# Kernel tuning notes

Hardware: AMD Instinct MI355X
Metric: run time of the kernel (lower is better)

## Reference

```python
import jax, jax.numpy as jnp
import numpy as np

D_MODEL = 1024
EXPAND = 2
D_INNER = D_MODEL * EXPAND  # 2048
C = 8
B, T = 4, 2048


def setup_inputs() -> dict:
    key = jax.random.key(0)
    ks = jax.random.split(key, 8)
    x = jax.random.normal(ks[0], (B, T, D_MODEL), jnp.float32)
    # omega init: uniform in [a, b] per the torch code
    a = np.log(1.0 / np.exp(np.log(0.999) / C) - 1.0)
    b = np.log(1.0 / np.exp(np.log(0.9) / C) - 1.0)
    omega = (a + (b - a) * jax.random.uniform(ks[1], (1, 1, D_INNER))).astype(jnp.float32)
    s = 0.02
    Win = (jax.random.normal(ks[2], (2 * D_INNER, D_MODEL)) * s).astype(jnp.float32)   # in_proj, no bias
    Wl = (jax.random.normal(ks[3], (D_INNER, D_INNER)) * s).astype(jnp.float32)        # lambda_proj weight
    bl = jnp.zeros((D_INNER,), jnp.float32)                                            # lambda_proj bias
    Wv = (jax.random.normal(ks[4], (D_INNER, D_INNER)) * s).astype(jnp.float32)        # mixer householder-vector proj
    bv = jnp.zeros((D_INNER,), jnp.float32)
    Wout = (jax.random.normal(ks[5], (D_MODEL, D_INNER)) * s).astype(jnp.float32)      # out_proj, no bias
    return dict(x=x, omega=omega, Win=Win, Wl=Wl, bl=bl, Wv=Wv, bv=bv, Wout=Wout)


def reference(x, omega, Win, Wl, bl, Wv, bv, Wout):
    # in_proj then split into (x, z)
    xz = jnp.einsum('btd,ed->bte', x, Win)              # [B,T,2*D_INNER]
    xi, z = jnp.split(xz, 2, axis=-1)                   # each [B,T,D_INNER]
    # lambda gate (computed for all timesteps at once)
    log_lam = -C * jax.nn.softplus(omega) * jax.nn.sigmoid(jnp.einsum('bti,ji->btj', xi, Wl) + bl)
    lam = jnp.exp(log_lam)                              # [B,T,D_INNER]
    # Householder (rank-1, identity activation) mixer vectors, hoisted out of the scan
    v = jnp.einsum('bti,ji->btj', xi, Wv) + bv          # [B,T,D_INNER]

    h0 = xi[:, 0]                                       # [B,D_INNER]

    def step(h_prev, inp):
        x_t, v_t, lam_t = inp
        vh = jnp.sum(v_t * h_prev, axis=-1, keepdims=True)
        vv = jnp.sum(v_t * v_t, axis=-1, keepdims=True)
        Qh = h_prev - 2.0 * v_t * (vh / vv)             # Householder reflection of h
        h = lam_t * Qh + (1.0 - lam_t) * x_t
        return h, h

    xs = (jnp.swapaxes(xi[:, 1:], 0, 1),                # [T-1,B,D_INNER]
          jnp.swapaxes(v[:, 1:], 0, 1),
          jnp.swapaxes(lam[:, 1:], 0, 1))
    _, hs = jax.lax.scan(step, h0, xs)                  # [T-1,B,D_INNER]
    h = jnp.concatenate([h0[:, None], jnp.swapaxes(hs, 0, 1)], axis=1)  # [B,T,D_INNER]

    return jnp.einsum('bti,di->btd', jax.nn.silu(z) * h, Wout)
```

## Files before the change

### kernel.cpp

```cpp
#include <hip/hip_runtime.h>
#include <cstdint>
#include <cstddef>

typedef unsigned short u16;
typedef __attribute__((ext_vector_type(8))) short s8v;
typedef __attribute__((ext_vector_type(4))) float f4v;
typedef __attribute__((ext_vector_type(2))) float f32x2;

#define D_MODEL 1024
#define D_INNER 2048
#define BT      8192
#define TLEN    2048
#define NBATCH  4

struct alignas(8) U16x4 { u16 x, y, z, w; };

__device__ __forceinline__ u16 f2bf(float f) {
  union { float f; unsigned u; } c; c.f = f;
  unsigned r = c.u + 0x7FFFu + ((c.u >> 16) & 1u);
  return (u16)(r >> 16);
}
__device__ __forceinline__ float blo(unsigned u) {
  union { unsigned u; float f; } c; c.u = u << 16; return c.f;
}
__device__ __forceinline__ float bhi(unsigned u) {
  union { unsigned u; float f; } c; c.u = u & 0xffff0000u; return c.f;
}
__device__ __forceinline__ unsigned pkbf(float lo, float hi) {
  union { float f; unsigned u; } a, b; a.f = lo; b.f = hi;
#if __has_builtin(__builtin_amdgcn_perm)
  return __builtin_amdgcn_perm(b.u + 0x8000u, a.u + 0x8000u, 0x07060302u);
#else
  return ((b.u + 0x8000u) & 0xffff0000u) | ((a.u + 0x8000u) >> 16);
#endif
}

#define DPPADD(x, ctrl) \
  ((x) + __builtin_bit_cast(float, __builtin_amdgcn_update_dpp( \
       0, __builtin_bit_cast(int, (x)), (ctrl), 0xF, 0xF, true)))
__device__ __forceinline__ float wave_sum_dpp(float x) {
  x = DPPADD(x, 0x111);
  x = DPPADD(x, 0x112);
  x = DPPADD(x, 0x114);
  x = DPPADD(x, 0x118);
  x = DPPADD(x, 0x142);
  x = DPPADD(x, 0x143);
  return x;
}

__device__ __forceinline__ void glds16(const u16* g, const u16* lds) {
  __builtin_amdgcn_global_load_lds(
      (const __attribute__((address_space(1))) unsigned int*)(uintptr_t)g,
      (__attribute__((address_space(3))) unsigned int*)(unsigned int)(uintptr_t)lds,
      16, 0, 0);
}

template<int EPI>
__global__ __launch_bounds__(256, 2)
void gemm_nt(const u16* __restrict__ A, const u16* __restrict__ B,
             int M, int N, int K,
             float* __restrict__ Cf, u16* __restrict__ Cb, u16* __restrict__ Cb2,
             const float* __restrict__ bias, const float* __restrict__ sfac,
             const float* __restrict__ bias2)
{
  __shared__ u16 lA[128 * 32];
  __shared__ u16 lB[128 * 32];
  const int tid  = threadIdx.x;
  const int wave = tid >> 6, lane = tid & 63;
  const int wm = wave >> 1, wn = wave & 1;

  const int nwg = (int)(gridDim.x * gridDim.y);
  int wg = (int)(blockIdx.y * gridDim.x + blockIdx.x);
  wg = (wg & 7) * (nwg >> 3) + (wg >> 3);
  const int bm0 = (wg / (int)gridDim.x) * 128;
  const int bn0 = (wg % (int)gridDim.x) * 128;

  const int srow = lane >> 2;
  const int scol = (lane & 3) * 8;
  const u16* pa0 = A + (size_t)(bm0 + wave * 32 + srow) * K + scol;
  const u16* pa1 = pa0 + (size_t)16 * K;
  const u16* pb0 = B + (size_t)(bn0 + wave * 32 + srow) * K + scol;
  const u16* pb1 = pb0 + (size_t)16 * K;
  u16* la0 = lA + (wave * 32) * 32;
  u16* la1 = la0 + 16 * 32;
  u16* lb0 = lB + (wave * 32) * 32;
  u16* lb1 = lb0 + 16 * 32;

  const int fr = lane & 15, kq = lane >> 4;
  const u16* fA = lA + (wm * 64 + fr) * 32 + kq * 8;
  const u16* fB = lB + (wn * 64 + fr) * 32 + kq * 8;

  f4v acc[4][4];
  const f4v zf = {0.f, 0.f, 0.f, 0.f};
  for (int i = 0; i < 4; ++i)
    for (int j = 0; j < 4; ++j)
      acc[i][j] = zf;

  for (int k0 = 0; k0 < K; k0 += 32) {
    glds16(pa0 + k0, la0);
    glds16(pa1 + k0, la1);
    glds16(pb0 + k0, lb0);
    glds16(pb1 + k0, lb1);
    __syncthreads();
    s8v af[4], bfv[4];
#pragma unroll
    for (int i = 0; i < 4; ++i) af[i] = *(const s8v*)(fA + i * 16 * 32);
#pragma unroll
    for (int j = 0; j < 4; ++j) bfv[j] = *(const s8v*)(fB + j * 16 * 32);
#pragma unroll
    for (int i = 0; i < 4; ++i)
#pragma unroll
      for (int j = 0; j < 4; ++j)
        acc[i][j] = __builtin_amdgcn_mfma_f32_16x16x32_bf16(af[i], bfv[j], acc[i][j], 0, 0, 0);
    __syncthreads();
  }

#pragma unroll
  for (int i = 0; i < 4; ++i) {
#pragma unroll
    for (int j = 0; j < 4; ++j) {
#pragma unroll
      for (int r = 0; r < 4; ++r) {
        const int gm = bm0 + wm * 64 + i * 16 + kq * 4 + r;
        const int gn = bn0 + wn * 64 + j * 16 + fr;
        const float val = acc[i][j][r];
        if (EPI == 0) {
          if (gn < D_INNER) {
            Cb[(size_t)gm * D_INNER + gn] = f2bf(val);
          } else {
            const float s = val / (1.f + __expf(-val));
            Cb2[(size_t)gm * D_INNER + (gn - D_INNER)] = f2bf(s);
          }
        } else if (EPI == 4) {
          if (gn < D_INNER) {
            const float pre = val + bias[gn];
            const float sig = 1.f / (1.f + __expf(-pre));
            const float m = -expm1f(sfac[gn] * sig);
            Cb2[(size_t)gm * D_INNER + gn] = f2bf(m);
          } else {
            Cb[(size_t)gm * D_INNER + (gn - D_INNER)] = f2bf(val + bias2[gn - D_INNER]);
          }
        } else {
          Cf[(size_t)gm * N + gn] = val;
        }
      }
    }
  }
}

#define CV_R0 2097152
#define CV_R1 3145728
#define CV_R2 4194304
#define CV_R3 5242880
#define CV_R4 5767168

__global__ __launch_bounds__(256)
void convall_kernel(const float* __restrict__ x, const float* __restrict__ Win,
                    const float* __restrict__ Wl, const float* __restrict__ Wv,
                    const float* __restrict__ Wout, u16* __restrict__ outb)
{
  const int g = blockIdx.x * 256 + threadIdx.x;
  const float* in; int lo;
  if (g < CV_R0)      { in = x;    lo = g; }
  else if (g < CV_R1) { in = Win;  lo = g - CV_R0; }
  else if (g < CV_R2) { in = Wl;   lo = g - CV_R1; }
  else if (g < CV_R3) { in = Wv;   lo = g - CV_R2; }
  else                { in = Wout; lo = g - CV_R3; }
  const float4 v = ((const float4*)in)[lo];
  U16x4 o; o.x = f2bf(v.x); o.y = f2bf(v.y); o.z = f2bf(v.z); o.w = f2bf(v.w);
  ((U16x4*)outb)[g] = o;
}

__global__ void sfac_kernel(const float* __restrict__ omega, float* __restrict__ sfac)
{
  const int i = blockIdx.x * blockDim.x + threadIdx.x;
  if (i < D_INNER) sfac[i] = -8.f * log1pf(expf(omega[i]));
}

__global__ __launch_bounds__(256)
void vscale_kernel(u16* __restrict__ v)
{
  const int row  = blockIdx.x * 4 + (threadIdx.x >> 6);
  const int lane = threadIdx.x & 63;
  uint4* p = (uint4*)(v + (size_t)row * D_INNER + lane * 32);
  uint4 a[4];
#pragma unroll
  for (int i = 0; i < 4; ++i) a[i] = p[i];
  float s = 0.f;
#pragma unroll
  for (int i = 0; i < 4; ++i) {
    const unsigned w[4] = {a[i].x, a[i].y, a[i].z, a[i].w};
#pragma unroll
    for (int j = 0; j < 4; ++j) {
      const float f0 = blo(w[j]), f1 = bhi(w[j]);
      s += f0 * f0 + f1 * f1;
    }
  }
  s += __shfl_down(s, 32); s += __shfl_down(s, 16); s += __shfl_down(s, 8);
  s += __shfl_down(s, 4);  s += __shfl_down(s, 2);  s += __shfl_down(s, 1);
  const float sc = sqrtf(2.f / __shfl(s, 0));
#pragma unroll
  for (int i = 0; i < 4; ++i) {
    const unsigned w[4] = {a[i].x, a[i].y, a[i].z, a[i].w};
    unsigned o[4];
#pragma unroll
    for (int j = 0; j < 4; ++j) o[j] = pkbf(blo(w[j]) * sc, bhi(w[j]) * sc);
    uint4 ov; ov.x = o[0]; ov.y = o[1]; ov.z = o[2]; ov.w = o[3];
    p[i] = ov;
  }
}

__global__ __launch_bounds__(256)
void pairprep_kernel(const u16* __restrict__ vs, const u16* __restrict__ mb,
                     const u16* __restrict__ xi, f32x2* __restrict__ C12)
{
  const int r = blockIdx.x * 4 + (threadIdx.x >> 6);
  const int lane = threadIdx.x & 63;
  const int b = r >> 10;
  const int t = (r & 1023) * 2;
  const size_t o0 = ((size_t)b * TLEN + t) * D_INNER + (size_t)lane * 32;
  const size_t o1 = o0 + D_INNER;
  const uint4* pv0 = (const uint4*)(vs + o0);
  const uint4* pv1 = (const uint4*)(vs + o1);
  const uint4* px0 = (const uint4*)(xi + o0);
  const uint4* pm0 = (const uint4*)(mb + o0);
  float c1 = 0.f, c2 = 0.f;
#pragma unroll
  for (int i = 0; i < 4; ++i) {
    const uint4 v0 = pv0[i], v1 = pv1[i], x0 = px0[i], m0 = pm0[i];
    const unsigned v0w[4] = {v0.x, v0.y, v0.z, v0.w};
    const unsigned v1w[4] = {v1.x, v1.y, v1.z, v1.w};
    const unsigned x0w[4] = {x0.x, x0.y, x0.z, x0.w};
    const unsigned m0w[4] = {m0.x, m0.y, m0.z, m0.w};
#pragma unroll
    for (int q = 0; q < 4; ++q) {
      const float va = blo(v0w[q]), vb = bhi(v0w[q]);
      const float ua = blo(v1w[q]), ub = bhi(v1w[q]);
      const float xa = blo(x0w[q]), xb = bhi(x0w[q]);
      const float ma = blo(m0w[q]), mbv = bhi(m0w[q]);
      const float wa = __builtin_fmaf(-ua, ma, ua);
      const float wb = __builtin_fmaf(-ub, mbv, ub);
      c1 += wa * va + wb * vb;
      c2 += ua * (ma * xa) + ub * (mbv * xb);
    }
  }
  c1 = wave_sum_dpp(c1);
  c2 = wave_sum_dpp(c2);
  if (lane == 63) { f32x2 cc; cc.x = c1; cc.y = c2; C12[r] = cc; }
}

__global__ void zmul_kernel(u16* __restrict__ gh, const u16* __restrict__ sz, int n8)
{
  const int i = blockIdx.x * blockDim.x + threadIdx.x;
  if (i >= n8) return;
  const uint4 hv = ((const uint4*)gh)[i];
  const uint4 zv = ((const uint4*)sz)[i];
  const unsigned hw[4] = {hv.x, hv.y, hv.z, hv.w};
  const unsigned zw[4] = {zv.x, zv.y, zv.z, zv.w};
  unsigned ow[4];
#pragma unroll
  for (int q = 0; q < 4; ++q)
    ow[q] = pkbf(blo(zw[q]) * blo(hw[q]), bhi(zw[q]) * bhi(hw[q]));
  uint4 o; o.x = ow[0]; o.y = ow[1]; o.z = ow[2]; o.w = ow[3];
  ((uint4*)gh)[i] = o;
}

struct Pair {
  uint4 v0, v1, x0, x1, m0, m1;
  f32x2 c;
};

__global__ __launch_bounds__(256, 1)
void scan2_kernel(const u16* __restrict__ xi, const u16* __restrict__ vs,
                  const u16* __restrict__ mb, const f32x2* __restrict__ C12,
                  u16* __restrict__ hb)
{
  const int b = blockIdx.x, tid = threadIdx.x;
  const int wave = tid >> 6, lane = tid & 63;
  const size_t base = (size_t)b * TLEN * D_INNER + (size_t)tid * 8;
  const int cb0 = b * 1024;
  __shared__ __attribute__((aligned(16))) float rP[2][4], rQ[2][4];

  auto load_pair = [&](int t) {
    Pair p;
    const size_t o0 = base + (size_t)t * D_INNER;
    const size_t o1 = o0 + D_INNER;
    p.v0 = *(const uint4*)(vs + o0);
    p.v1 = *(const uint4*)(vs + o1);
    p.x0 = *(const uint4*)(xi + o0);
    p.x1 = *(const uint4*)(xi + o1);
    p.m0 = *(const uint4*)(mb + o0);
    p.m1 = *(const uint4*)(mb + o1);
    p.c = C12[cb0 + (t >> 1)];
    return p;
  };

  float h[8];
  {
    const uint4 x0 = *(const uint4*)(xi + base);
    const unsigned xw[4] = {x0.x, x0.y, x0.z, x0.w};
#pragma unroll
    for (int p = 0; p < 4; ++p) {
      h[2*p]   = blo(xw[p]);
      h[2*p+1] = bhi(xw[p]);
    }
    *(uint4*)(hb + base) = x0;
  }

  {
    const size_t o = base + D_INNER;
    const uint4 v1v = *(const uint4*)(vs + o);
    const uint4 x1v = *(const uint4*)(xi + o);
    const uint4 m1v = *(const uint4*)(mb + o);
    const unsigned vw[4] = {v1v.x, v1v.y, v1v.z, v1v.w};
    float vf[8];
    float P0 = 0.f, P1 = 0.f;
#pragma unroll
    for (int p = 0; p < 4; ++p) {
      vf[2*p]   = blo(vw[p]);
      vf[2*p+1] = bhi(vw[p]);
      P0 = __builtin_fmaf(vf[2*p],   h[2*p],   P0);
      P1 = __builtin_fmaf(vf[2*p+1], h[2*p+1], P1);
    }
    float P = wave_sum_dpp(P0 + P1);
    if (lane == 63) rP[0][wave] = P;
    asm volatile("s_waitcnt lgkmcnt(0)\n\ts_barrier" ::: "memory");
    const float4 sp = *(const float4*)rP[0];
    const float a = (sp.x + sp.y) + (sp.z + sp.w);
    const unsigned xw[4] = {x1v.x, x1v.y, x1v.z, x1v.w};
    const unsigned mw[4] = {m1v.x, m1v.y, m1v.z, m1v.w};
    unsigned ow[4];
#pragma unroll
    for (int p = 0; p < 4; ++p) {
      const float X0 = blo(xw[p]), X1 = bhi(xw[p]);
      const float M0 = blo(mw[p]), M1 = bhi(mw[p]);
      const float t0 = __builtin_fmaf(vf[2*p],   -a, h[2*p]);
      const float t1 = __builtin_fmaf(vf[2*p+1], -a, h[2*p+1]);
      h[2*p]   = __builtin_fmaf(M0, X0 - t0, t0);
      h[2*p+1] = __builtin_fmaf(M1, X1 - t1, t1);
      ow[p] = pkbf(h[2*p], h[2*p+1]);
    }
    uint4 out; out.x = ow[0]; out.y = ow[1]; out.z = ow[2]; out.w = ow[3];
    *(uint4*)(hb + o) = out;
  }

  auto round = [&](const Pair& p, int t) {
    const int par = (t >> 1) & 1;
    const unsigned v0w[4] = {p.v0.x, p.v0.y, p.v0.z, p.v0.w};
    const unsigned v1w[4] = {p.v1.x, p.v1.y, p.v1.z, p.v1.w};
    const unsigned m0w[4] = {p.m0.x, p.m0.y, p.m0.z, p.m0.w};
    float vf[8], uf[8], mf0[8];
    float P0 = 0.f, P1 = 0.f, Q0 = 0.f, Q1 = 0.f;
#pragma unroll
    for (int q = 0; q < 4; ++q) {
      vf[2*q]   = blo(v0w[q]);
      vf[2*q+1] = bhi(v0w[q]);
      uf[2*q]   = blo(v1w[q]);
      uf[2*q+1] = bhi(v1w[q]);
      mf0[2*q]  = blo(m0w[q]);
      mf0[2*q+1]= bhi(m0w[q]);
      const float wa = __builtin_fmaf(-uf[2*q],   mf0[2*q],   uf[2*q]);
      const float wb = __builtin_fmaf(-uf[2*q+1], mf0[2*q+1], uf[2*q+1]);
      P0 = __builtin_fmaf(vf[2*q],   h[2*q],   P0);
      P1 = __builtin_fmaf(vf[2*q+1], h[2*q+1], P1);
      Q0 = __builtin_fmaf(wa, h[2*q],   Q0);
      Q1 = __builtin_fmaf(wb, h[2*q+1], Q1);
    }
    float P = wave_sum_dpp(P0 + P1);
    float Q = wave_sum_dpp(Q0 + Q1);
    if (lane == 63) { rP[par][wave] = P; rQ[par][wave] = Q; }
    asm volatile("s_waitcnt lgkmcnt(0)\n\ts_barrier" ::: "memory");
    const float4 sp = *(const float4*)rP[par];
    const float4 sq = *(const float4*)rQ[par];
    const float a0 = (sp.x + sp.y) + (sp.z + sp.w);
    const float a1 = __builtin_fmaf(-a0, p.c.x, (sq.x + sq.y) + (sq.z + sq.w) + p.c.y);
    const unsigned xw0[4] = {p.x0.x, p.x0.y, p.x0.z, p.x0.w};
    const unsigned xw1[4] = {p.x1.x, p.x1.y, p.x1.z, p.x1.w};
    const unsigned m1w[4] = {p.m1.x, p.m1.y, p.m1.z, p.m1.w};
    unsigned ow0[4], ow1[4];
#pragma unroll
    for (int q = 0; q < 4; ++q) {
      const float A0 = blo(xw0[q]), A1 = bhi(xw0[q]);
      const float B0 = blo(xw1[q]), B1 = bhi(xw1[q]);
      const float N0 = blo(m1w[q]), N1 = bhi(m1w[q]);
      float t0 = __builtin_fmaf(vf[2*q],   -a0, h[2*q]);
      float t1 = __builtin_fmaf(vf[2*q+1], -a0, h[2*q+1]);
      t0 = __builtin_fmaf(mf0[2*q],   A0 - t0, t0);
      t1 = __builtin_fmaf(mf0[2*q+1], A1 - t1, t1);
      ow0[q] = pkbf(t0, t1);
      const float u0 = __builtin_fmaf(uf[2*q],   -a1, t0);
      const float u1 = __builtin_fmaf(uf[2*q+1], -a1, t1);
      h[2*q]   = __builtin_fmaf(N0, B0 - u0, u0);
      h[2*q+1] = __builtin_fmaf(N1, B1 - u1, u1);
      ow1[q] = pkbf(h[2*q], h[2*q+1]);
    }
    const size_t oo = base + (size_t)t * D_INNER;
    uint4 o0; o0.x = ow0[0]; o0.y = ow0[1]; o0.z = ow0[2]; o0.w = ow0[3];
    uint4 o1; o1.x = ow1[0]; o1.y = ow1[1]; o1.z = ow1[2]; o1.w = ow1[3];
    *(uint4*)(hb + oo) = o0;
    *(uint4*)(hb + oo + D_INNER) = o1;
  };

  Pair A = load_pair(2);
  __builtin_amdgcn_sched_barrier(0);
  Pair B = load_pair(4);
  __builtin_amdgcn_sched_barrier(0);
  for (int t = 2; t <= 2038; t += 4) {
    Pair An = load_pair(t + 4);
    __builtin_amdgcn_sched_barrier(0);
    round(A, t);
    A = An;
    Pair Bn = load_pair(t + 6);
    __builtin_amdgcn_sched_barrier(0);
    round(B, t + 2);
    B = Bn;
  }
  {
    Pair An = load_pair(2046);
    __builtin_amdgcn_sched_barrier(0);
    round(A, 2042);
    round(B, 2044);
    round(An, 2046);
  }
}

extern "C" void kernel_launch(void* const* d_in, const int* in_sizes, int n_in,
                              void* d_out, int out_size, void* d_ws, size_t ws_size,
                              hipStream_t stream)
{
  const float* x     = (const float*)d_in[0];
  const float* omega = (const float*)d_in[1];
  const float* Win   = (const float*)d_in[2];
  const float* Wl    = (const float*)d_in[3];
  const float* bl    = (const float*)d_in[4];
  const float* Wv    = (const float*)d_in[5];
  const float* bv    = (const float*)d_in[6];
  const float* Wout  = (const float*)d_in[7];
  float* out = (float*)d_out;
  (void)in_sizes; (void)n_in; (void)out_size; (void)ws_size;

  size_t off = 0;
  auto carve = [&](size_t bytes) -> void* {
    void* r = (char*)d_ws + off;
    off += (bytes + 255) & ~(size_t)255;
    return r;
  };
  u16*  x_bf    = (u16*)carve((size_t)BT * D_MODEL * 2);
  u16*  Win_bf  = (u16*)carve((size_t)2 * D_INNER * D_MODEL * 2);
  u16*  Wl_bf   = (u16*)carve((size_t)D_INNER * D_INNER * 2);
  u16*  Wv_bf   = (u16*)carve((size_t)D_INNER * D_INNER * 2);
  u16*  Wout_bf = (u16*)carve((size_t)D_MODEL * D_INNER * 2);
  u16*  xi_bf   = (u16*)carve((size_t)BT * D_INNER * 2);
  u16*  sz_bf   = (u16*)carve((size_t)BT * D_INNER * 2);
  u16*  v_bf    = (u16*)carve((size_t)BT * D_INNER * 2);
  u16*  gh_bf   = (u16*)carve((size_t)BT * D_INNER * 2);
  u16*  mb      = (u16*)carve((size_t)BT * D_INNER * 2);
  float* sfac   = (float*)carve((size_t)D_INNER * 4);
  f32x2* C12    = (f32x2*)carve((size_t)(BT / 2) * 8);

  convall_kernel<<<CV_R4 / 256, 256, 0, stream>>>(x, Win, Wl, Wv, Wout, x_bf);
  sfac_kernel<<<(D_INNER + 255) / 256, 256, 0, stream>>>(omega, sfac);

  gemm_nt<0><<<dim3(4096 / 128, BT / 128), 256, 0, stream>>>(
      x_bf, Win_bf, BT, 4096, D_MODEL, nullptr, xi_bf, sz_bf, nullptr, nullptr, nullptr);
  gemm_nt<4><<<dim3(4096 / 128, BT / 128), 256, 0, stream>>>(
      xi_bf, Wl_bf, BT, 4096, D_INNER, nullptr, v_bf, mb, bl, sfac, bv);
  vscale_kernel<<<BT / 4, 256, 0, stream>>>(v_bf);
  pairprep_kernel<<<BT / 2 / 4, 256, 0, stream>>>(v_bf, mb, xi_bf, C12);
  scan2_kernel<<<NBATCH, 256, 0, stream>>>(xi_bf, v_bf, mb, C12, gh_bf);
  zmul_kernel<<<(BT * D_INNER / 8 + 255) / 256, 256, 0, stream>>>(gh_bf, sz_bf, BT * D_INNER / 8);
  gemm_nt<3><<<dim3(D_MODEL / 128, BT / 128), 256, 0, stream>>>(
      gh_bf, Wout_bf, BT, D_MODEL, D_INNER, out, nullptr, nullptr, nullptr, nullptr, nullptr);
}
```

Before: 1.070 ms.

## Widen GEMM K-tile, fuse v normalization into pair prep, deepen scan prefetch

The bf16 GEMM now stages a 64-wide K slice per iteration, two MFMA sub-steps between barriers instead of one, using twice the LDS. The separate v normalization kernel is merged into the pair-prep kernel, which scales both rows of each pair and writes them back before computing the pair coefficients, saving one read pass and a launch. The sequential scan keeps three pairs of timesteps in flight instead of two to hide more global-load latency, at the cost of more registers.

```diff
diff --git a/kernel.cpp b/kernel.cpp
--- a/kernel.cpp
+++ b/kernel.cpp
@@ -63,8 +63,8 @@
              const float* __restrict__ bias, const float* __restrict__ sfac,
              const float* __restrict__ bias2)
 {
-  __shared__ u16 lA[128 * 32];
-  __shared__ u16 lB[128 * 32];
+  __shared__ u16 lA[128 * 64];
+  __shared__ u16 lB[128 * 64];
   const int tid  = threadIdx.x;
   const int wave = tid >> 6, lane = tid & 63;
   const int wm = wave >> 1, wn = wave & 1;
@@ -75,20 +75,16 @@
   const int bm0 = (wg / (int)gridDim.x) * 128;
   const int bn0 = (wg % (int)gridDim.x) * 128;
 
-  const int srow = lane >> 2;
-  const int scol = (lane & 3) * 8;
-  const u16* pa0 = A + (size_t)(bm0 + wave * 32 + srow) * K + scol;
-  const u16* pa1 = pa0 + (size_t)16 * K;
-  const u16* pb0 = B + (size_t)(bn0 + wave * 32 + srow) * K + scol;
-  const u16* pb1 = pb0 + (size_t)16 * K;
-  u16* la0 = lA + (wave * 32) * 32;
-  u16* la1 = la0 + 16 * 32;
-  u16* lb0 = lB + (wave * 32) * 32;
-  u16* lb1 = lb0 + 16 * 32;
+  const int srow = lane >> 3;
+  const int scol = (lane & 7) * 8;
+  const u16* pa = A + (size_t)(bm0 + wave * 32 + srow) * K + scol;
+  const u16* pb = B + (size_t)(bn0 + wave * 32 + srow) * K + scol;
+  u16* laB = lA + (wave * 32) * 64;
+  u16* lbB = lB + (wave * 32) * 64;
 
   const int fr = lane & 15, kq = lane >> 4;
-  const u16* fA = lA + (wm * 64 + fr) * 32 + kq * 8;
-  const u16* fB = lB + (wn * 64 + fr) * 32 + kq * 8;
+  const u16* fA = lA + (wm * 64 + fr) * 64 + kq * 8;
+  const u16* fB = lB + (wn * 64 + fr) * 64 + kq * 8;
 
   f4v acc[4][4];
   const f4v zf = {0.f, 0.f, 0.f, 0.f};
@@ -96,22 +92,26 @@
     for (int j = 0; j < 4; ++j)
       acc[i][j] = zf;
 
-  for (int k0 = 0; k0 < K; k0 += 32) {
-    glds16(pa0 + k0, la0);
-    glds16(pa1 + k0, la1);
-    glds16(pb0 + k0, lb0);
-    glds16(pb1 + k0, lb1);
+  for (int k0 = 0; k0 < K; k0 += 64) {
+#pragma unroll
+    for (int g = 0; g < 4; ++g) {
+      glds16(pa + (size_t)(8 * g) * K + k0, laB + (8 * g) * 64);
+      glds16(pb + (size_t)(8 * g) * K + k0, lbB + (8 * g) * 64);
+    }
     __syncthreads();
-    s8v af[4], bfv[4];
-#pragma unroll
-    for (int i = 0; i < 4; ++i) af[i] = *(const s8v*)(fA + i * 16 * 32);
-#pragma unroll
-    for (int j = 0; j < 4; ++j) bfv[j] = *(const s8v*)(fB + j * 16 * 32);
-#pragma unroll
-    for (int i = 0; i < 4; ++i)
-#pragma unroll
-      for (int j = 0; j < 4; ++j)
-        acc[i][j] = __builtin_amdgcn_mfma_f32_16x16x32_bf16(af[i], bfv[j], acc[i][j], 0, 0, 0);
+#pragma unroll
+    for (int ks = 0; ks < 2; ++ks) {
+      s8v af[4], bfv[4];
+#pragma unroll
+      for (int i = 0; i < 4; ++i) af[i] = *(const s8v*)(fA + i * 16 * 64 + ks * 32);
+#pragma unroll
+      for (int j = 0; j < 4; ++j) bfv[j] = *(const s8v*)(fB + j * 16 * 64 + ks * 32);
+#pragma unroll
+      for (int i = 0; i < 4; ++i)
+#pragma unroll
+        for (int j = 0; j < 4; ++j)
+          acc[i][j] = __builtin_amdgcn_mfma_f32_16x16x32_bf16(af[i], bfv[j], acc[i][j], 0, 0, 0);
+    }
     __syncthreads();
   }
 
@@ -178,41 +178,8 @@
 }
 
 __global__ __launch_bounds__(256)
-void vscale_kernel(u16* __restrict__ v)
-{
-  const int row  = blockIdx.x * 4 + (threadIdx.x >> 6);
-  const int lane = threadIdx.x & 63;
-  uint4* p = (uint4*)(v + (size_t)row * D_INNER + lane * 32);
-  uint4 a[4];
-#pragma unroll
-  for (int i = 0; i < 4; ++i) a[i] = p[i];
-  float s = 0.f;
-#pragma unroll
-  for (int i = 0; i < 4; ++i) {
-    const unsigned w[4] = {a[i].x, a[i].y, a[i].z, a[i].w};
-#pragma unroll
-    for (int j = 0; j < 4; ++j) {
-      const float f0 = blo(w[j]), f1 = bhi(w[j]);
-      s += f0 * f0 + f1 * f1;
-    }
-  }
-  s += __shfl_down(s, 32); s += __shfl_down(s, 16); s += __shfl_down(s, 8);
-  s += __shfl_down(s, 4);  s += __shfl_down(s, 2);  s += __shfl_down(s, 1);
-  const float sc = sqrtf(2.f / __shfl(s, 0));
-#pragma unroll
-  for (int i = 0; i < 4; ++i) {
-    const unsigned w[4] = {a[i].x, a[i].y, a[i].z, a[i].w};
-    unsigned o[4];
-#pragma unroll
-    for (int j = 0; j < 4; ++j) o[j] = pkbf(blo(w[j]) * sc, bhi(w[j]) * sc);
-    uint4 ov; ov.x = o[0]; ov.y = o[1]; ov.z = o[2]; ov.w = o[3];
-    p[i] = ov;
-  }
-}
-
-__global__ __launch_bounds__(256)
-void pairprep_kernel(const u16* __restrict__ vs, const u16* __restrict__ mb,
-                     const u16* __restrict__ xi, f32x2* __restrict__ C12)
+void prep_kernel(u16* __restrict__ vs, const u16* __restrict__ mb,
+                 const u16* __restrict__ xi, f32x2* __restrict__ C12)
 {
   const int r = blockIdx.x * 4 + (threadIdx.x >> 6);
   const int lane = threadIdx.x & 63;
@@ -220,22 +187,55 @@
   const int t = (r & 1023) * 2;
   const size_t o0 = ((size_t)b * TLEN + t) * D_INNER + (size_t)lane * 32;
   const size_t o1 = o0 + D_INNER;
-  const uint4* pv0 = (const uint4*)(vs + o0);
-  const uint4* pv1 = (const uint4*)(vs + o1);
+  uint4* pv0 = (uint4*)(vs + o0);
+  uint4* pv1 = (uint4*)(vs + o1);
   const uint4* px0 = (const uint4*)(xi + o0);
   const uint4* pm0 = (const uint4*)(mb + o0);
+
+  uint4 a0[4], a1[4];
+  float s0 = 0.f, s1 = 0.f;
+#pragma unroll
+  for (int i = 0; i < 4; ++i) {
+    a0[i] = pv0[i]; a1[i] = pv1[i];
+    const unsigned w0[4] = {a0[i].x, a0[i].y, a0[i].z, a0[i].w};
+    const unsigned w1[4] = {a1[i].x, a1[i].y, a1[i].z, a1[i].w};
+#pragma unroll
+    for (int j = 0; j < 4; ++j) {
+      const float f0 = blo(w0[j]), f1 = bhi(w0[j]);
+      s0 += f0 * f0 + f1 * f1;
+      const float g0 = blo(w1[j]), g1 = bhi(w1[j]);
+      s1 += g0 * g0 + g1 * g1;
+    }
+  }
+  s0 += __shfl_down(s0, 32); s0 += __shfl_down(s0, 16); s0 += __shfl_down(s0, 8);
+  s0 += __shfl_down(s0, 4);  s0 += __shfl_down(s0, 2);  s0 += __shfl_down(s0, 1);
+  s1 += __shfl_down(s1, 32); s1 += __shfl_down(s1, 16); s1 += __shfl_down(s1, 8);
+  s1 += __shfl_down(s1, 4);  s1 += __shfl_down(s1, 2);  s1 += __shfl_down(s1, 1);
+  const float sc0 = sqrtf(2.f / __shfl(s0, 0));
+  const float sc1 = sqrtf(2.f / __shfl(s1, 0));
+
   float c1 = 0.f, c2 = 0.f;
 #pragma unroll
   for (int i = 0; i < 4; ++i) {
-    const uint4 v0 = pv0[i], v1 = pv1[i], x0 = px0[i], m0 = pm0[i];
-    const unsigned v0w[4] = {v0.x, v0.y, v0.z, v0.w};
-    const unsigned v1w[4] = {v1.x, v1.y, v1.z, v1.w};
+    const unsigned w0[4] = {a0[i].x, a0[i].y, a0[i].z, a0[i].w};
+    const unsigned w1[4] = {a1[i].x, a1[i].y, a1[i].z, a1[i].w};
+    unsigned ow0[4], ow1[4];
+#pragma unroll
+    for (int j = 0; j < 4; ++j) {
+      ow0[j] = pkbf(blo(w0[j]) * sc0, bhi(w0[j]) * sc0);
+      ow1[j] = pkbf(blo(w1[j]) * sc1, bhi(w1[j]) * sc1);
+    }
+    uint4 v0o; v0o.x = ow0[0]; v0o.y = ow0[1]; v0o.z = ow0[2]; v0o.w = ow0[3];
+    uint4 v1o; v1o.x = ow1[0]; v1o.y = ow1[1]; v1o.z = ow1[2]; v1o.w = ow1[3];
+    pv0[i] = v0o;
+    pv1[i] = v1o;
+    const uint4 m0 = pm0[i], x0 = px0[i];
+    const unsigned m0w[4] = {m0.x, m0.y, m0.z, m0.w};
     const unsigned x0w[4] = {x0.x, x0.y, x0.z, x0.w};
-    const unsigned m0w[4] = {m0.x, m0.y, m0.z, m0.w};
 #pragma unroll
     for (int q = 0; q < 4; ++q) {
-      const float va = blo(v0w[q]), vb = bhi(v0w[q]);
-      const float ua = blo(v1w[q]), ub = bhi(v1w[q]);
+      const float va = blo(ow0[q]), vb = bhi(ow0[q]);
+      const float ua = blo(ow1[q]), ub = bhi(ow1[q]);
       const float xa = blo(x0w[q]), xb = bhi(x0w[q]);
       const float ma = blo(m0w[q]), mbv = bhi(m0w[q]);
       const float wa = __builtin_fmaf(-ua, ma, ua);
@@ -405,23 +405,25 @@
   __builtin_amdgcn_sched_barrier(0);
   Pair B = load_pair(4);
   __builtin_amdgcn_sched_barrier(0);
-  for (int t = 2; t <= 2038; t += 4) {
-    Pair An = load_pair(t + 4);
+  Pair C = load_pair(6);
+  __builtin_amdgcn_sched_barrier(0);
+  for (int t = 2; t <= 2036; t += 6) {
+    Pair An = load_pair(t + 6);
     __builtin_amdgcn_sched_barrier(0);
     round(A, t);
     A = An;
-    Pair Bn = load_pair(t + 6);
+    Pair Bn = load_pair(t + 8);
     __builtin_amdgcn_sched_barrier(0);
     round(B, t + 2);
     B = Bn;
-  }
-  {
-    Pair An = load_pair(2046);
+    Pair Cn = load_pair(t + 10);
     __builtin_amdgcn_sched_barrier(0);
-    round(A, 2042);
-    round(B, 2044);
-    round(An, 2046);
-  }
+    round(C, t + 4);
+    C = Cn;
+  }
+  round(A, 2042);
+  round(B, 2044);
+  round(C, 2046);
 }
 
 extern "C" void kernel_launch(void* const* d_in, const int* in_sizes, int n_in,
@@ -465,8 +467,7 @@
       x_bf, Win_bf, BT, 4096, D_MODEL, nullptr, xi_bf, sz_bf, nullptr, nullptr, nullptr);
   gemm_nt<4><<<dim3(4096 / 128, BT / 128), 256, 0, stream>>>(
       xi_bf, Wl_bf, BT, 4096, D_INNER, nullptr, v_bf, mb, bl, sfac, bv);
-  vscale_kernel<<<BT / 4, 256, 0, stream>>>(v_bf);
-  pairprep_kernel<<<BT / 2 / 4, 256, 0, stream>>>(v_bf, mb, xi_bf, C12);
+  prep_kernel<<<BT / 2 / 4, 256, 0, stream>>>(v_bf, mb, xi_bf, C12);
   scan2_kernel<<<NBATCH, 256, 0, stream>>>(xi_bf, v_bf, mb, C12, gh_bf);
   zmul_kernel<<<(BT * D_INNER / 8 + 255) / 256, 256, 0, stream>>>(gh_bf, sz_bf, BT * D_INNER / 8);
   gemm_nt<3><<<dim3(D_MODEL / 128, BT / 128), 256, 0, stream>>>(
```

Measured after the change: 1.104 ms. 3.2% more time.
